# Kernel optimization log

Hardware: AMD Instinct MI355X
Metric: run time of the kernel (lower is better)

Reference implementation:

```python
import jax, jax.numpy as jnp
import numpy as np

NUM_GROUPS = 32
EPS = 1e-6


def group_norm(x, gamma, beta):
    # x: (B, C, H, W)
    B, C, H, W = x.shape
    g = x.reshape(B, NUM_GROUPS, C // NUM_GROUPS, H, W)
    mean = g.mean(axis=(2, 3, 4), keepdims=True)
    var = g.var(axis=(2, 3, 4), keepdims=True)
    g = (g - mean) / jnp.sqrt(var + EPS)
    g = g.reshape(B, C, H, W)
    return g * gamma[None, :, None, None] + beta[None, :, None, None]


def nin(x, W, b):
    # 1x1 linear projection over channel dim
    return jnp.einsum('bchw,cd->bdhw', x, W) + b[None, :, None, None]


def setup_inputs() -> dict:
    key = jax.random.key(0)
    ks = jax.random.split(key, 8)
    B, C, H, W = 32, 512, 32, 32
    lim = np.sqrt(3 * 0.1 / C)  # NIN init_scale=0.1 uniform limit
    return {
        'x': jax.random.normal(ks[0], (B, C, H, W), jnp.float32),
        'gamma': jnp.ones((C,), jnp.float32),
        'beta': jnp.zeros((C,), jnp.float32),
        'Wq': jax.random.uniform(ks[1], (C, C), jnp.float32, -lim, lim),
        'bq': jnp.zeros((C,), jnp.float32),
        'Wk': jax.random.uniform(ks[2], (C, C), jnp.float32, -lim, lim),
        'bk': jnp.zeros((C,), jnp.float32),
        'Wv': jax.random.uniform(ks[3], (C, C), jnp.float32, -lim, lim),
        'bv': jnp.zeros((C,), jnp.float32),
        'Wp': jax.random.normal(ks[4], (C, C), jnp.float32) * 1e-5,  # init_scale=0.0 -> ~0
        'bp': jnp.zeros((C,), jnp.float32),
    }


def reference(x, gamma, beta, Wq, bq, Wk, bk, Wv, bv, Wp, bp):
    B, C, H, W = x.shape
    h = group_norm(x, gamma, beta)
    q = nin(h, Wq, bq)
    k = nin(h, Wk, bk)
    v = nin(h, Wv, bv)
    # full (HW)x(HW) attention weights, as the original materializes
    w = jnp.einsum('bchw,bcHW->bhwHW', q, k) * (C ** -0.5)
    w = w.reshape(B, H, W, H * W)
    w = jax.nn.softmax(w, axis=-1)
    w = w.reshape(B, H, W, H, W)
    h_out = jnp.einsum('bhwHW,bcHW->bchw', w, v)
    h_out = nin(h_out, Wp, bp)
    return x + h_out
```

## Files before the change

kernel.cpp:

```cpp
#include <hip/hip_runtime.h>
#include <hip/hip_bf16.h>
#include <math.h>

typedef __attribute__((ext_vector_type(8))) short bf16x8;
typedef __attribute__((ext_vector_type(4))) float f32x4;

typedef const __attribute__((address_space(1))) unsigned int guint;
typedef __attribute__((address_space(3))) unsigned int luint;

static __device__ __forceinline__ short f2bf(float f) {
    union { float f; unsigned u; } a; a.f = f;
    unsigned r = 0x7FFFu + ((a.u >> 16) & 1u);
    return (short)((a.u + r) >> 16);
}
static __device__ __forceinline__ float bf2f(short s) {
    union { unsigned u; float f; } a;
    a.u = ((unsigned)(unsigned short)s) << 16;
    return a.f;
}

__global__ __launch_bounds__(256)
void transpose_w(const float* __restrict__ w0, const float* __restrict__ w1,
                 const float* __restrict__ w2, const float* __restrict__ w3,
                 short* __restrict__ outT, float qscale)
{
    __shared__ float ld[32][33];
    const float* W = (blockIdx.z == 0) ? w0 : (blockIdx.z == 1) ? w1
                   : (blockIdx.z == 2) ? w2 : w3;
    const float sc = (blockIdx.z == 0) ? qscale : 1.f;
    short* O = outT + (long long)blockIdx.z * 512 * 512;
    const int tx = threadIdx.x & 31, ty = threadIdx.x >> 5;
    const int c0 = blockIdx.y * 32, d0 = blockIdx.x * 32;
#pragma unroll
    for (int r = 0; r < 4; ++r)
        ld[ty + 8 * r][tx] = W[(long long)(c0 + ty + 8 * r) * 512 + d0 + tx];
    __syncthreads();
#pragma unroll
    for (int r = 0; r < 4; ++r)
        O[(long long)(d0 + ty + 8 * r) * 512 + c0 + tx] = f2bf(ld[tx][ty + 8 * r] * sc);
}

__global__ __launch_bounds__(256)
void concat_bias(const float* __restrict__ bq, const float* __restrict__ bk,
                 float* __restrict__ bqk, float qscale)
{
    int i = blockIdx.x * 256 + threadIdx.x;
    bqk[i] = (i < 512) ? bq[i] * qscale : bk[i - 512];
}

__global__ __launch_bounds__(256)
void gn_fused(const float* __restrict__ x, const float* __restrict__ gamma,
              const float* __restrict__ beta, short* __restrict__ hn)
{
    __shared__ float xs[16 * 1024];
    __shared__ float red[256];
    const int bg = blockIdx.x;
    const int g  = bg & 31;
    const int t  = threadIdx.x;
    const float4* px = reinterpret_cast<const float4*>(x + (long long)bg * 16384);
    float s = 0.f, ss = 0.f;
#pragma unroll
    for (int i = 0; i < 16; ++i) {
        float4 v = px[t + 256 * i];
        reinterpret_cast<float4*>(xs)[t + 256 * i] = v;
        s  += v.x + v.y + v.z + v.w;
        ss += v.x * v.x + v.y * v.y + v.z * v.z + v.w * v.w;
    }
    red[t] = s; __syncthreads();
    for (int o = 128; o > 0; o >>= 1) {
        if (t < o) red[t] += red[t + o];
        __syncthreads();
    }
    const float mean = red[0] * (1.f / 16384.f);
    __syncthreads();
    red[t] = ss; __syncthreads();
    for (int o = 128; o > 0; o >>= 1) {
        if (t < o) red[t] += red[t + o];
        __syncthreads();
    }
    const float var  = red[0] * (1.f / 16384.f) - mean * mean;
    const float rstd = rsqrtf(var + 1e-6f);

    const int half = t & 1;
    float ga[8], be[8];
#pragma unroll
    for (int cc = 0; cc < 8; ++cc) {
        ga[cc] = gamma[g * 16 + half * 8 + cc];
        be[cc] = beta[g * 16 + half * 8 + cc];
    }
    short* out = hn + (long long)bg * 16384;
#pragma unroll
    for (int it = 0; it < 8; ++it) {
        const int sidx = it * 128 + (t >> 1);
        bf16x8 o;
#pragma unroll
        for (int cc = 0; cc < 8; ++cc) {
            float v = xs[(half * 8 + cc) * 1024 + sidx];
            o[cc] = f2bf((v - mean) * rstd * ga[cc] + be[cc]);
        }
        *reinterpret_cast<bf16x8*>(out + sidx * 16 + half * 8) = o;
    }
}

template<int BIAS_M, int BIAS_N, int RESID, int EXPRS, int DIVROW4, int HN_A, int HN_B>
__global__ __launch_bounds__(512, 1)
void nt_gemm(const short* __restrict__ A, const short* __restrict__ B,
             void* __restrict__ Cv,
             const float* __restrict__ biasM, const float* __restrict__ biasN,
             const float* __restrict__ resid, float* __restrict__ rs,
             float scale, int K, int lda, int ldb, int ldc,
             long long sA, long long sB, long long sC,
             int tilesM, int tilesPerBatch)
{
    __shared__ short lsA[2][2][128 * 64];
    __shared__ short lsB[2][2][128 * 64];

    const int id = blockIdx.x;
    const int chunk = gridDim.x >> 3;
    const int gid = (id & 7) * chunk + (id >> 3);
    const int bz = gid / tilesPerBatch;
    const int tt = gid - bz * tilesPerBatch;
    const int m0 = (tt % tilesM) * 256;
    const int n0 = (tt / tilesM) * 256;

    const int t = threadIdx.x;
    const int lane = t & 63;
    const int w = t >> 6;
    const int wrs = w >> 1;
    const int wcs = w & 1;
    const int lr16 = lane & 15, lkg = lane >> 4;
    const int sw = lr16 & 7;

    const int srow = t >> 3;
    const int jch  = (t & 7) ^ (srow & 7);
    const int scol = jch * 8;

    const short* gA; int rsA, ktA;
    if (HN_A) {
        gA = A + ((long long)bz * 32 + (jch >> 1)) * 16384
               + (long long)(m0 + srow) * 16 + (jch & 1) * 8;
        rsA = 16; ktA = 65536;
    } else {
        gA = A + (long long)bz * sA + (long long)(m0 + srow) * lda + scol;
        rsA = lda; ktA = 64;
    }
    const short* gB; int rsB, ktB;
    if (HN_B) {
        gB = B + ((long long)bz * 32 + (jch >> 1)) * 16384
               + (long long)(n0 + srow) * 16 + (jch & 1) * 8;
        rsB = 16; ktB = 65536;
    } else {
        gB = B + (long long)bz * sB + (long long)(n0 + srow) * ldb + scol;
        rsB = ldb; ktB = 64;
    }

    f32x4 acc[4][2][4];
#pragma unroll
    for (int q = 0; q < 4; ++q)
#pragma unroll
        for (int i = 0; i < 2; ++i)
#pragma unroll
            for (int j = 0; j < 4; ++j) acc[q][i][j] = (f32x4){0.f, 0.f, 0.f, 0.f};

    const int nk = K >> 6;

#define STAGE_A(buf, h, kt)                                                    \
    {                                                                          \
        _Pragma("unroll")                                                      \
        for (int c = 0; c < 2; ++c)                                            \
            __builtin_amdgcn_global_load_lds(                                  \
                (guint*)(gA + (long long)(kt) * ktA                            \
                            + (long long)((h) * 128 + 64 * c) * rsA),          \
                (luint*)&lsA[buf][h][t * 8 + 4096 * c], 16, 0, 0);             \
    }
#define STAGE_B(buf, h, kt)                                                    \
    {                                                                          \
        _Pragma("unroll")                                                      \
        for (int c = 0; c < 2; ++c)                                            \
            __builtin_amdgcn_global_load_lds(                                  \
                (guint*)(gB + (long long)(kt) * ktB                            \
                            + (long long)((h) * 128 + 64 * c) * rsB),          \
                (luint*)&lsB[buf][h][t * 8 + 4096 * c], 16, 0, 0);             \
    }

#define LDA_HALF(dst, buf, h)                                                  \
    _Pragma("unroll")                                                          \
    for (int mi2 = 0; mi2 < 2; ++mi2)                                          \
        _Pragma("unroll")                                                      \
        for (int ks = 0; ks < 2; ++ks)                                         \
            dst[mi2][ks] = *reinterpret_cast<const bf16x8*>(                   \
                &lsA[buf][h][(wrs * 32 + mi2 * 16 + lr16) * 64 +               \
                             (((ks * 4 + lkg) ^ sw) * 8)]);
#define LDB_HALF(dst, buf, h)                                                  \
    _Pragma("unroll")                                                          \
    for (int ni = 0; ni < 4; ++ni)                                             \
        _Pragma("unroll")                                                      \
        for (int ks = 0; ks < 2; ++ks)                                         \
            dst[ni][ks] = *reinterpret_cast<const bf16x8*>(                    \
                &lsB[buf][h][(wcs * 64 + ni * 16 + lr16) * 64 +                \
                             (((ks * 4 + lkg) ^ sw) * 8)]);

#define MFMAQ(q, Af, Bf)                                                       \
    _Pragma("unroll")                                                          \
    for (int ks = 0; ks < 2; ++ks)                                             \
        _Pragma("unroll")                                                      \
        for (int mi2 = 0; mi2 < 2; ++mi2)                                      \
            _Pragma("unroll")                                                  \
            for (int ni = 0; ni < 4; ++ni)                                     \
                acc[q][mi2][ni] = __builtin_amdgcn_mfma_f32_16x16x32_bf16(     \
                    Af[mi2][ks], Bf[ni][ks], acc[q][mi2][ni], 0, 0, 0);

#define PH_END(N)                                                              \
    asm volatile("s_waitcnt vmcnt(" #N ")" ::: "memory");                      \
    __builtin_amdgcn_s_barrier();                                              \
    __builtin_amdgcn_sched_barrier(0)

#define FRAME(b, kt)                                                           \
    {                                                                          \
        bf16x8 a0[2][2], a1[2][2], b0f[4][2], b1f[4][2];                       \
           \
        LDB_HALF(b0f, b, 0)                                                    \
        LDA_HALF(a0, b, 0)                                                     \
        LDB_HALF(b1f, b, 1)                                                    \
        STAGE_B((b) ^ 1, 0, (kt) + 1);                                         \
        STAGE_B((b) ^ 1, 1, (kt) + 1);                                         \
        STAGE_A((b) ^ 1, 0, (kt) + 1);                                         \
        MFMAQ(0, a0, b0f)                                                      \
        MFMAQ(1, a0, b1f)                                                      \
        PH_END(6);                                                             \
              \
        LDA_HALF(a1, b, 1)                                                     \
        STAGE_A((b) ^ 1, 1, (kt) + 1);                                         \
        MFMAQ(2, a1, b0f)                                                      \
        MFMAQ(3, a1, b1f)                                                      \
        PH_END(2);                                                             \
    }

    STAGE_B(0, 0, 0); STAGE_B(0, 1, 0); STAGE_A(0, 0, 0);
    STAGE_A(0, 1, 0);
    PH_END(2);

    for (int kt = 0; kt < nk; kt += 2) {
        FRAME(0, kt)
        FRAME(1, kt + 1)
    }
#undef STAGE_A
#undef STAGE_B
#undef LDA_HALF
#undef LDB_HALF
#undef MFMAQ
#undef PH_END
#undef FRAME

    float psum[2][2][4];
    if (EXPRS) {
#pragma unroll
        for (int ah = 0; ah < 2; ++ah)
#pragma unroll
            for (int mi2 = 0; mi2 < 2; ++mi2)
#pragma unroll
                for (int j = 0; j < 4; ++j) psum[ah][mi2][j] = 0.f;
    }
#pragma unroll
    for (int ah = 0; ah < 2; ++ah) {
#pragma unroll
        for (int bh = 0; bh < 2; ++bh) {
#pragma unroll
            for (int mi2 = 0; mi2 < 2; ++mi2) {
                float addm[4], mul[4];
#pragma unroll
                for (int j = 0; j < 4; ++j) {
                    const int rrow = m0 + ah * 128 + wrs * 32 + mi2 * 16 + lkg * 4 + j;
                    addm[j] = BIAS_M ? biasM[rrow] : 0.f;
                    if (DIVROW4) {
                        const float* r4 = rs + (long long)bz * 4096 + rrow;
                        mul[j] = 1.f / (r4[0] + r4[1024] + r4[2048] + r4[3072]);
                    } else mul[j] = 1.f;
                }
#pragma unroll
                for (int ni = 0; ni < 4; ++ni) {
                    const int col = n0 + bh * 128 + wcs * 64 + ni * 16 + lr16;
                    float bn = BIAS_N ? biasN[col] : 0.f;
#pragma unroll
                    for (int j = 0; j < 4; ++j) {
                        const int rrow = m0 + ah * 128 + wrs * 32 + mi2 * 16 + lkg * 4 + j;
                        float v2 = acc[ah * 2 + bh][mi2][ni][j] + addm[j] + bn;
                        v2 *= scale;
                        if (EXPRS) { v2 = __expf(v2 - 8.f); psum[ah][mi2][j] += v2; }
                        if (DIVROW4) v2 *= mul[j];
                        const long long idx = (long long)rrow * ldc + col;
                        if (RESID) {
                            float* Cf = (float*)Cv + (long long)bz * sC;
                            Cf[idx] = v2 + resid[(long long)bz * sC + idx];
                        } else {
                            short* Cs = (short*)Cv + (long long)bz * sC;
                            Cs[idx] = f2bf(v2);
                        }
                    }
                }
            }
        }
    }
    if (EXPRS) {
#pragma unroll
        for (int ah = 0; ah < 2; ++ah)
#pragma unroll
            for (int mi2 = 0; mi2 < 2; ++mi2)
#pragma unroll
                for (int j = 0; j < 4; ++j) {
                    float v = psum[ah][mi2][j];
                    v += __shfl_xor(v, 1); v += __shfl_xor(v, 2);
                    v += __shfl_xor(v, 4); v += __shfl_xor(v, 8);
                    psum[ah][mi2][j] = v;
                }
        float* scr = (float*)&lsA[1][0][0];
        __syncthreads();
        if (lr16 == 0) {
#pragma unroll
            for (int ah = 0; ah < 2; ++ah)
#pragma unroll
                for (int mi2 = 0; mi2 < 2; ++mi2)
#pragma unroll
                    for (int j = 0; j < 4; ++j)
                        scr[wcs * 256 + ah * 128 + wrs * 32 + mi2 * 16 + lkg * 4 + j]
                            = psum[ah][mi2][j];
        }
        __syncthreads();
        if (t < 256)
            rs[(long long)bz * 4096 + (n0 >> 8) * 1024 + m0 + t]
                = scr[t] + scr[256 + t];
    }
}

extern "C" void kernel_launch(void* const* d_in, const int* in_sizes, int n_in,
                              void* d_out, int out_size, void* d_ws, size_t ws_size,
                              hipStream_t stream)
{
    (void)in_sizes; (void)n_in; (void)out_size; (void)ws_size;
    const float* x     = (const float*)d_in[0];
    const float* gamma = (const float*)d_in[1];
    const float* beta  = (const float*)d_in[2];
    const float* Wq = (const float*)d_in[3];
    const float* bq = (const float*)d_in[4];
    const float* Wk = (const float*)d_in[5];
    const float* bk = (const float*)d_in[6];
    const float* Wv = (const float*)d_in[7];
    const float* bv = (const float*)d_in[8];
    const float* Wp = (const float*)d_in[9];
    const float* bp = (const float*)d_in[10];
    float* out = (float*)d_out;

    char* ws = (char*)d_ws;
    short*  expS = (short*)ws;
    short*  hn   = (short*)ws;
    short*  qkb  = (short*)(ws + (64LL << 20));
    short*  vbuf = (short*)(ws + (128LL << 20));
    short*  wT   = (short*)(ws + (160LL << 20));
    float*  bqk  = (float*)(ws + (162LL << 20) + (16 << 10));
    float*  rs4  = (float*)(ws + (162LL << 20) + (32 << 10));
    short*  ho   = qkb;

    const short* WqkT = wT;
    const short* WvT  = wT + 2 * 512 * 512;
    const short* WpT  = wT + 3 * 512 * 512;

    const float qscale = 0.044194173824159216f;

    transpose_w<<<dim3(16, 16, 4), 256, 0, stream>>>(Wq, Wk, Wv, Wp, wT, qscale);
    concat_bias<<<dim3(4), 256, 0, stream>>>(bq, bk, bqk, qscale);
    gn_fused<<<dim3(1024), 256, 0, stream>>>(x, gamma, beta, hn);

    nt_gemm<0, 1, 0, 0, 0, 1, 0><<<512, 512, 0, stream>>>(
        hn, WqkT, qkb, nullptr, bqk, nullptr, nullptr, 1.f,
        512, 512, 512, 1024, 0, 0, 1024LL * 1024, 4, 16);
    nt_gemm<1, 0, 0, 0, 0, 0, 1><<<256, 512, 0, stream>>>(
        WvT, hn, vbuf, bv, nullptr, nullptr, nullptr, 1.f,
        512, 512, 512, 1024, 0, 0, 512 * 1024, 2, 8);
    nt_gemm<0, 0, 0, 1, 0, 0, 0><<<512, 512, 0, stream>>>(
        qkb, qkb + 512, expS, nullptr, nullptr, nullptr, rs4, 1.f,
        512, 1024, 1024, 1024, 1024LL * 1024, 1024LL * 1024, 1024LL * 1024, 4, 16);
    nt_gemm<0, 0, 0, 0, 1, 0, 0><<<256, 512, 0, stream>>>(
        expS, vbuf, ho, nullptr, nullptr, nullptr, rs4, 1.f,
        1024, 1024, 1024, 512, 1024LL * 1024, 512 * 1024, 1024 * 512, 4, 8);
    nt_gemm<1, 0, 1, 0, 0, 0, 0><<<256, 512, 0, stream>>>(
        WpT, ho, out, bp, nullptr, x, nullptr, 1.f,
        512, 512, 512, 1024, 0, 1024 * 512, 512LL * 1024, 2, 8);
}
```

Before: 201.9 us.

## Fold Q/K and V/P projection weights into combined matrices to drop GEMMs

Restructures the attention algebra: precomputes Wq·Wk^T (scaled) and Wv·Wp as 512x512 matrices, so scores become hn·M·hn^T plus a per-column bias term, and the output becomes (P·hn)·(WvWp) plus a folded bias. This removes the separate V projection and halves the QK projection width. The combined weights are built with small GEMM launches each call, and a transposed hn copy is emitted by the group-norm kernel. Folding the weights before rounding to bf16 changes where rounding error enters, and the extra small kernels add launch overhead.

```diff
diff --git a/kernel.cpp b/kernel.cpp
--- a/kernel.cpp
+++ b/kernel.cpp
@@ -17,6 +17,21 @@
     union { unsigned u; float f; } a;
     a.u = ((unsigned)(unsigned short)s) << 16;
     return a.f;
+}
+
+__global__ __launch_bounds__(256)
+void cast_w3(const float* __restrict__ wq, const float* __restrict__ wk,
+             const float* __restrict__ wv, short* __restrict__ out)
+{
+    const float* W = (blockIdx.y == 0) ? wq : (blockIdx.y == 1) ? wk : wv;
+    short* O = out + (long long)blockIdx.y * 262144;
+    int i = (blockIdx.x * 256 + threadIdx.x) * 8;
+    float4 a = *reinterpret_cast<const float4*>(W + i);
+    float4 b = *reinterpret_cast<const float4*>(W + i + 4);
+    bf16x8 o;
+    o[0] = f2bf(a.x); o[1] = f2bf(a.y); o[2] = f2bf(a.z); o[3] = f2bf(a.w);
+    o[4] = f2bf(b.x); o[5] = f2bf(b.y); o[6] = f2bf(b.z); o[7] = f2bf(b.w);
+    *reinterpret_cast<bf16x8*>(O + i) = o;
 }
 
 __global__ __launch_bounds__(256)
@@ -41,21 +56,40 @@
 }
 
 __global__ __launch_bounds__(256)
-void concat_bias(const float* __restrict__ bq, const float* __restrict__ bk,
-                 float* __restrict__ bqk, float qscale)
-{
-    int i = blockIdx.x * 256 + threadIdx.x;
-    bqk[i] = (i < 512) ? bq[i] * qscale : bk[i - 512];
+void vec_pre(const float* __restrict__ Wp, const float* __restrict__ bp,
+             const float* __restrict__ bv, const float* __restrict__ Wk,
+             const float* __restrict__ bq, float* __restrict__ b2,
+             float* __restrict__ wkbq)
+{
+    const int t = threadIdx.x;
+    if (blockIdx.x == 0) {
+#pragma unroll
+        for (int r = 0; r < 2; ++r) {
+            int d2 = t * 2 + r;
+            float a = bp[d2];
+            for (int d = 0; d < 512; ++d) a += bv[d] * Wp[d * 512 + d2];
+            b2[d2] = a;
+        }
+    } else {
+#pragma unroll
+        for (int r = 0; r < 2; ++r) {
+            int c = t * 2 + r;
+            float a = 0.f;
+            for (int d = 0; d < 512; ++d) a += Wk[c * 512 + d] * bq[d];
+            wkbq[c] = a;
+        }
+    }
 }
 
 __global__ __launch_bounds__(256)
 void gn_fused(const float* __restrict__ x, const float* __restrict__ gamma,
-              const float* __restrict__ beta, short* __restrict__ hn)
+              const float* __restrict__ beta, short* __restrict__ hn,
+              short* __restrict__ hnT)
 {
     __shared__ float xs[16 * 1024];
     __shared__ float red[256];
     const int bg = blockIdx.x;
-    const int g  = bg & 31;
+    const int g  = bg & 31, b = bg >> 5;
     const int t  = threadIdx.x;
     const float4* px = reinterpret_cast<const float4*>(x + (long long)bg * 16384);
     float s = 0.f, ss = 0.f;
@@ -88,7 +122,7 @@
         ga[cc] = gamma[g * 16 + half * 8 + cc];
         be[cc] = beta[g * 16 + half * 8 + cc];
     }
-    short* out = hn + (long long)bg * 16384;
+    short* outB = hn + (long long)bg * 16384;
 #pragma unroll
     for (int it = 0; it < 8; ++it) {
         const int sidx = it * 128 + (t >> 1);
@@ -98,11 +132,34 @@
             float v = xs[(half * 8 + cc) * 1024 + sidx];
             o[cc] = f2bf((v - mean) * rstd * ga[cc] + be[cc]);
         }
-        *reinterpret_cast<bf16x8*>(out + sidx * 16 + half * 8) = o;
-    }
-}
-
-template<int BIAS_M, int BIAS_N, int RESID, int EXPRS, int DIVROW4, int HN_A, int HN_B>
+        *reinterpret_cast<bf16x8*>(outB + sidx * 16 + half * 8) = o;
+    }
+    short* oT = hnT + ((long long)b * 512 + g * 16) * 1024;
+#pragma unroll
+    for (int cc = 0; cc < 16; ++cc) {
+        const float g_ = gamma[g * 16 + cc], b_ = beta[g * 16 + cc];
+        const int pos = t * 4;
+        short4 o4;
+        o4.x = f2bf((xs[cc * 1024 + pos + 0] - mean) * rstd * g_ + b_);
+        o4.y = f2bf((xs[cc * 1024 + pos + 1] - mean) * rstd * g_ + b_);
+        o4.z = f2bf((xs[cc * 1024 + pos + 2] - mean) * rstd * g_ + b_);
+        o4.w = f2bf((xs[cc * 1024 + pos + 3] - mean) * rstd * g_ + b_);
+        *reinterpret_cast<short4*>(oT + cc * 1024 + pos) = o4;
+    }
+}
+
+__global__ __launch_bounds__(256)
+void colv_k(const short* __restrict__ hnT, const float* __restrict__ wkbq,
+            float* __restrict__ colv, float qs)
+{
+    const int b = blockIdx.y, j = blockIdx.x * 256 + threadIdx.x;
+    const short* p = hnT + (long long)b * 512 * 1024 + j;
+    float a = 0.f;
+    for (int c = 0; c < 512; ++c) a += wkbq[c] * bf2f(p[c * 1024]);
+    colv[b * 1024 + j] = a * qs;
+}
+
+template<int BIAS_M, int BIAS_NB, int RESID, int EXPRS, int DIVROW4, int HN_A, int HN_B>
 __global__ __launch_bounds__(512, 1)
 void nt_gemm(const short* __restrict__ A, const short* __restrict__ B,
              void* __restrict__ Cv,
@@ -117,7 +174,7 @@
 
     const int id = blockIdx.x;
     const int chunk = gridDim.x >> 3;
-    const int gid = (id & 7) * chunk + (id >> 3);
+    const int gid = chunk ? ((id & 7) * chunk + (id >> 3)) : id;
     const int bz = gid / tilesPerBatch;
     const int tt = gid - bz * tilesPerBatch;
     const int m0 = (tt % tilesM) * 256;
@@ -218,7 +275,6 @@
 #define FRAME(b, kt)                                                           \
     {                                                                          \
         bf16x8 a0[2][2], a1[2][2], b0f[4][2], b1f[4][2];                       \
-           \
         LDB_HALF(b0f, b, 0)                                                    \
         LDA_HALF(a0, b, 0)                                                     \
         LDB_HALF(b1f, b, 1)                                                    \
@@ -228,7 +284,6 @@
         MFMAQ(0, a0, b0f)                                                      \
         MFMAQ(1, a0, b1f)                                                      \
         PH_END(6);                                                             \
-              \
         LDA_HALF(a1, b, 1)                                                     \
         STAGE_A((b) ^ 1, 1, (kt) + 1);                                         \
         MFMAQ(2, a1, b0f)                                                      \
@@ -280,7 +335,7 @@
 #pragma unroll
                 for (int ni = 0; ni < 4; ++ni) {
                     const int col = n0 + bh * 128 + wcs * 64 + ni * 16 + lr16;
-                    float bn = BIAS_N ? biasN[col] : 0.f;
+                    float bn = BIAS_NB ? biasN[(long long)bz * 1024 + col] : 0.f;
 #pragma unroll
                     for (int j = 0; j < 4; ++j) {
                         const int rrow = m0 + ah * 128 + wrs * 32 + mi2 * 16 + lkg * 4 + j;
@@ -343,7 +398,7 @@
     const float* Wq = (const float*)d_in[3];
     const float* bq = (const float*)d_in[4];
     const float* Wk = (const float*)d_in[5];
-    const float* bk = (const float*)d_in[6];
+    const float* bk = (const float*)d_in[6];  (void)bk;
     const float* Wv = (const float*)d_in[7];
     const float* bv = (const float*)d_in[8];
     const float* Wp = (const float*)d_in[9];
@@ -351,38 +406,47 @@
     float* out = (float*)d_out;
 
     char* ws = (char*)d_ws;
+    short*  wq_bf  = (short*)ws;
+    short*  wk_bf  = wq_bf + 262144;
+    short*  wv_bf  = wq_bf + 2 * 262144;
+    short*  wpT_bf = wq_bf + 3 * 262144;
     short*  expS = (short*)ws;
-    short*  hn   = (short*)ws;
-    short*  qkb  = (short*)(ws + (64LL << 20));
-    short*  vbuf = (short*)(ws + (128LL << 20));
-    short*  wT   = (short*)(ws + (160LL << 20));
-    float*  bqk  = (float*)(ws + (162LL << 20) + (16 << 10));
-    float*  rs4  = (float*)(ws + (162LL << 20) + (32 << 10));
-    short*  ho   = qkb;
-
-    const short* WqkT = wT;
-    const short* WvT  = wT + 2 * 512 * 512;
-    const short* WpT  = wT + 3 * 512 * 512;
+    short*  hnT  = (short*)(ws + (64LL << 20));
+    short*  tmp  = (short*)(ws + (96LL << 20));
+    short*  hn   = (short*)(ws + (128LL << 20));
+    short*  MqkT = (short*)(ws + (160LL << 20));
+    short*  Avp  = MqkT + 262144;
+    float*  rs4  = (float*)(ws + (161LL << 20));
+    float*  colv = rs4 + 32 * 4096;
+    float*  b2   = colv + 32 * 1024;
+    float*  wkbq = b2 + 512;
+    short*  Phn  = tmp;
 
     const float qscale = 0.044194173824159216f;
 
-    transpose_w<<<dim3(16, 16, 4), 256, 0, stream>>>(Wq, Wk, Wv, Wp, wT, qscale);
-    concat_bias<<<dim3(4), 256, 0, stream>>>(bq, bk, bqk, qscale);
-    gn_fused<<<dim3(1024), 256, 0, stream>>>(x, gamma, beta, hn);
-
-    nt_gemm<0, 1, 0, 0, 0, 1, 0><<<512, 512, 0, stream>>>(
-        hn, WqkT, qkb, nullptr, bqk, nullptr, nullptr, 1.f,
-        512, 512, 512, 1024, 0, 0, 1024LL * 1024, 4, 16);
-    nt_gemm<1, 0, 0, 0, 0, 0, 1><<<256, 512, 0, stream>>>(
-        WvT, hn, vbuf, bv, nullptr, nullptr, nullptr, 1.f,
-        512, 512, 512, 1024, 0, 0, 512 * 1024, 2, 8);
-    nt_gemm<0, 0, 0, 1, 0, 0, 0><<<512, 512, 0, stream>>>(
-        qkb, qkb + 512, expS, nullptr, nullptr, nullptr, rs4, 1.f,
-        512, 1024, 1024, 1024, 1024LL * 1024, 1024LL * 1024, 1024LL * 1024, 4, 16);
+    cast_w3<<<dim3(128, 3), 256, 0, stream>>>(Wq, Wk, Wv, wq_bf);
+    transpose_w<<<dim3(16, 16, 1), 256, 0, stream>>>(Wp, Wp, Wp, Wp, wpT_bf, 1.f);
+    vec_pre<<<dim3(2), 256, 0, stream>>>(Wp, bp, bv, Wk, bq, b2, wkbq);
+    nt_gemm<0, 0, 0, 0, 0, 0, 0><<<4, 512, 0, stream>>>(
+        wk_bf, wq_bf, MqkT, nullptr, nullptr, nullptr, nullptr, qscale,
+        512, 512, 512, 512, 0, 0, 0, 2, 4);
+    nt_gemm<0, 0, 0, 0, 0, 0, 0><<<4, 512, 0, stream>>>(
+        wpT_bf, wv_bf, Avp, nullptr, nullptr, nullptr, nullptr, 1.f,
+        512, 512, 512, 512, 0, 0, 0, 2, 4);
+
+    gn_fused<<<dim3(1024), 256, 0, stream>>>(x, gamma, beta, hn, hnT);
+    colv_k<<<dim3(4, 32), 256, 0, stream>>>(hnT, wkbq, colv, qscale);
+
+    nt_gemm<0, 0, 0, 0, 0, 1, 0><<<256, 512, 0, stream>>>(
+        hn, MqkT, tmp, nullptr, nullptr, nullptr, nullptr, 1.f,
+        512, 0, 512, 512, 0, 0, 512LL * 1024, 4, 8);
+    nt_gemm<0, 1, 0, 1, 0, 0, 1><<<512, 512, 0, stream>>>(
+        tmp, hn, expS, nullptr, colv, nullptr, rs4, 1.f,
+        512, 512, 0, 1024, 512LL * 1024, 0, 1024LL * 1024, 4, 16);
     nt_gemm<0, 0, 0, 0, 1, 0, 0><<<256, 512, 0, stream>>>(
-        expS, vbuf, ho, nullptr, nullptr, nullptr, rs4, 1.f,
-        1024, 1024, 1024, 512, 1024LL * 1024, 512 * 1024, 1024 * 512, 4, 8);
+        expS, hnT, Phn, nullptr, nullptr, nullptr, rs4, 1.f,
+        1024, 1024, 1024, 512, 1024LL * 1024, 512LL * 1024, 512LL * 1024, 4, 8);
     nt_gemm<1, 0, 1, 0, 0, 0, 0><<<256, 512, 0, stream>>>(
-        WpT, ho, out, bp, nullptr, x, nullptr, 1.f,
-        512, 512, 512, 1024, 0, 1024 * 512, 512LL * 1024, 2, 8);
-}
+        Avp, Phn, out, b2, nullptr, x, nullptr, 1.f,
+        512, 512, 512, 1024, 0, 512LL * 1024, 512LL * 1024, 2, 8);
+}
```

New measurement: 262.3 us. 29.9% more time.
